# Performance work log

Measured on AMD Instinct MI355X. Metric: run time of the kernel, lower is better.

The kernel has to match this reference:

```python
import jax, jax.numpy as jnp
import numpy as np

MAX_SEQ_LEN = 8192
B, S, D = 4, 8192, 1024
H = 4  # attention heads
N_LEVELS = 3  # levels 1..3 actually occur in the lattice


def _build_spine(max_seq_len):
    spine = [0, 2, 4]
    while True:
        nv = 2 * spine[-1] + 2 * spine[-2] + 2 * spine[-3]
        if nv >= max_seq_len:
            break
        spine.append(nv)
    return spine


def _anc(spine, pos):
    # 3 immediate ancestors from the recurrence (only defined for spine idx >= 3)
    if pos in spine:
        i = spine.index(pos)
        if i >= 3:
            return [spine[i - 1], spine[i - 2], spine[i - 3]]
    return []


def _build_lattice(max_seq_len, seq_len):
    """Static lattice: per spine position, per level, (node indices, path-count weights)."""
    spine = _build_spine(max_seq_len)
    out = []
    for p in spine:
        if p < 3 or p >= seq_len:
            continue
        visited = {p}
        cur = [p]
        levels = {}
        lvl = 0
        while cur and lvl < 10:
            levels[lvl] = list(cur)
            nxt = set()
            for n in cur:
                for a in _anc(spine, n):
                    if a not in visited and a >= 0:
                        visited.add(a)
                        nxt.add(a)
            cur = sorted(nxt)
            lvl += 1
        max_depth = lvl - 1
        # path counts: #paths from p to each ancestor; deepest level pinned to 1 (as in source)
        pc = {p: 1}
        for L in range(1, max_depth + 1):
            for n in levels[L]:
                if L == max_depth:
                    pc[n] = 1
                else:
                    pc[n] = sum(pc.get(c, 0) for c in levels[L - 1] if n in _anc(spine, c))
        entries = []
        for L in range(1, max_depth + 1):
            nodes = [n for n in levels[L] if n < seq_len]
            if nodes:
                entries.append((L, np.asarray(nodes, np.int32),
                                np.asarray([pc.get(n, 1) for n in nodes], np.float32)))
        if entries:
            out.append((p, entries))
    return out


LATTICE = _build_lattice(MAX_SEQ_LEN, S)


def _ln(v, g, b, eps=1e-5):
    mu = jnp.mean(v, axis=-1, keepdims=True)
    var = jnp.mean((v - mu) ** 2, axis=-1, keepdims=True)
    return (v - mu) / jnp.sqrt(var + eps) * g + b


def setup_inputs() -> dict:
    key = jax.random.key(0)
    ks = jax.random.split(key, 10)
    s = 0.02
    return {
        "x": jax.random.normal(ks[0], (B, S, D), jnp.float32),
        # per-level MLP (levels 1..3), stacked: Linear -> LayerNorm -> GELU -> Linear
        "lt_w1": jax.random.normal(ks[1], (N_LEVELS, D, D), jnp.float32) * s,
        "lt_b1": jnp.zeros((N_LEVELS, D), jnp.float32),
        "lt_ln_g": jnp.ones((N_LEVELS, D), jnp.float32),
        "lt_ln_b": jnp.zeros((N_LEVELS, D), jnp.float32),
        "lt_w2": jax.random.normal(ks[2], (N_LEVELS, D, D), jnp.float32) * s,
        "lt_b2": jnp.zeros((N_LEVELS, D), jnp.float32),
        # MultiheadAttention (torch layout): in_proj [3D,D], out_proj [D,D]
        "attn_in_w": jax.random.normal(ks[3], (3 * D, D), jnp.float32) * s,
        "attn_in_b": jnp.zeros((3 * D,), jnp.float32),
        "attn_out_w": jax.random.normal(ks[4], (D, D), jnp.float32) * s,
        "attn_out_b": jnp.zeros((D,), jnp.float32),
        # fusion: Linear(2D->D) + LayerNorm
        "fus_w": jax.random.normal(ks[5], (D, 2 * D), jnp.float32) * s,
        "fus_b": jnp.zeros((D,), jnp.float32),
        "fus_ln_g": jnp.ones((D,), jnp.float32),
        "fus_ln_b": jnp.zeros((D,), jnp.float32),
    }


def reference(x, lt_w1, lt_b1, lt_ln_g, lt_ln_b, lt_w2, lt_b2,
              attn_in_w, attn_in_b, attn_out_w, attn_out_b,
              fus_w, fus_b, fus_ln_g, fus_ln_b):
    Bq, Sq, Dm = x.shape
    hd = Dm // H
    Wq, Wk, Wv = jnp.split(attn_in_w, 3, axis=0)
    bq, bk, bv = jnp.split(attn_in_b, 3)
    pos_list, upds = [], []
    for pos, entries in LATTICE:  # 7 static spine positions
        feats = []
        for (L, nodes, w) in entries:  # <=3 levels, <=3 nodes each
            g = x[:, jnp.asarray(nodes), :]                       # [B,k,D] gather
            wa = jnp.asarray(w)
            f = jnp.einsum('bkd,k->bd', g, wa) / wa.sum()          # weighted mean
            i = L - 1
            h = f @ lt_w1[i].T + lt_b1[i]
            h = _ln(h, lt_ln_g[i], lt_ln_b[i])
            h = jax.nn.gelu(h, approximate=False)
            feats.append(h @ lt_w2[i].T + lt_b2[i])
        kv = jnp.stack(feats, axis=1)                              # [B,L,D]
        q = x[:, pos]                                              # [B,D]
        qh = (q @ Wq.T + bq).reshape(Bq, H, hd)
        kh = (kv @ Wk.T + bk).reshape(Bq, -1, H, hd)
        vh = (kv @ Wv.T + bv).reshape(Bq, -1, H, hd)
        scores = jnp.einsum('bhd,blhd->bhl', qh, kh) / jnp.sqrt(jnp.float32(hd))
        att = jax.nn.softmax(scores, axis=-1)
        o = jnp.einsum('bhl,blhd->bhd', att, vh).reshape(Bq, Dm)
        o = o @ attn_out_w.T + attn_out_b
        comb = jnp.concatenate([o, q], axis=-1)                    # [B,2D]
        upds.append(_ln(comb @ fus_w.T + fus_b, fus_ln_g, fus_ln_b))
        pos_list.append(pos)
    # single scatter of all updated spine positions
    return x.at[:, jnp.asarray(pos_list, jnp.int32), :].set(jnp.stack(upds, axis=1))
```

## Files before the change

kernel.cpp:

```cpp
#include <hip/hip_runtime.h>
#include <math.h>


#define SEQ 8192
#define DM  1024

typedef float fx4 __attribute__((ext_vector_type(4)));

__device__ __constant__ int c_nodes[16][3] = {
  {0,2,4},{2,4,12},{4,12,36},{12,36,104},{36,104,304},{104,304,888},{304,888,2592},
  {0,0,0},{0,2,0},{0,2,4},{2,4,12},{4,12,36},{12,36,104},
  {0,0,0},{0,2,0},{0,2,4}};
__device__ __constant__ float c_wt[16][3] = {
  {1,1,1},{1,1,1},{1,1,1},{1,1,1},{1,1,1},{1,1,1},{1,1,1},
  {1,0,0},{1,1,0},{1,1,1},{1,2,3},{1,2,3},{1,2,3},
  {1,0,0},{1,1,0},{1,1,1}};
__device__ __constant__ float c_winv[16] = {
  1.f/3.f,1.f/3.f,1.f/3.f,1.f/3.f,1.f/3.f,1.f/3.f,1.f/3.f,
  1.f,0.5f,1.f/3.f,1.f/6.f,1.f/6.f,1.f/6.f,
  1.f,0.5f,1.f/3.f};
__device__ __constant__ int c_pos[7]  = {12,36,104,304,888,2592,7568};
__device__ __constant__ int c_ne[7]   = {1,2,2,2,3,3,3};
__device__ __constant__ int c_posE[7][3] = {
  {0,0,0},{1,7,0},{2,8,0},{3,9,0},{4,10,13},{5,11,14},{6,12,15}};

__device__ __constant__ int c_lr0[9]  = {0,8,16,24,28,36,44,52,60};
__device__ __constant__ int c_lnr[9]  = {8,8,8,4,8,8,8,8,4};
__device__ __constant__ int c_llv[9]  = {0,0,0,0,1,1,1,2,2};
__device__ __constant__ int c_or0[4]  = {0,8,16,24};
__device__ __constant__ int c_onr[4]  = {8,8,8,4};

__device__ __forceinline__ void copy4(const float* __restrict__ x,
                                      float* __restrict__ out, int c0)
{
  const fx4* __restrict__ src4 = (const fx4*)x;
  fx4* __restrict__ dst4 = (fx4*)out;
  const int tid = threadIdx.x;
  fx4 v[16]; size_t idx[16];
#pragma unroll
  for (int u = 0; u < 16; ++u) {
    const int c = c0 + (u >> 2), k = u & 3;
    idx[u] = (size_t)c * 1024 + (size_t)k * 256 + tid;
    v[u] = src4[idx[u]];
  }
#pragma unroll
  for (int u = 0; u < 16; ++u) {
    const int s = ((c0 + (u >> 2)) * 4 + (u & 3)) & (SEQ - 1);
    if (s==12 || s==36 || s==104 || s==304 || s==888 || s==2592 || s==7568)
      continue;
    __builtin_nontemporal_store(v[u], &dst4[idx[u]]);
  }
}

__device__ __forceinline__ void acc8(float (&A)[4][8],
                                     const float* const (&Xr)[8],
                                     const float* __restrict__ W,
                                     int Wld, int wcol, int j0, int T)
{
  const int lane = threadIdx.x & 63;
  for (int t = 0; t < T; ++t) {
    const int k = t * 256 + lane * 4;
    const float* wp = W + (size_t)j0 * Wld + wcol + k;
    const float4 w0 = *(const float4*)(wp);
    const float4 w1 = *(const float4*)(wp + Wld);
    const float4 w2 = *(const float4*)(wp + 2 * Wld);
    const float4 w3 = *(const float4*)(wp + 3 * Wld);
#pragma unroll
    for (int r = 0; r < 8; ++r) {
      const float4 xv = *(const float4*)(Xr[r] + k);
      A[0][r] += w0.x*xv.x + w0.y*xv.y + w0.z*xv.z + w0.w*xv.w;
      A[1][r] += w1.x*xv.x + w1.y*xv.y + w1.z*xv.z + w1.w*xv.w;
      A[2][r] += w2.x*xv.x + w2.y*xv.y + w2.z*xv.z + w2.w*xv.w;
      A[3][r] += w3.x*xv.x + w3.y*xv.y + w3.z*xv.z + w3.w*xv.w;
    }
  }
}

__device__ __forceinline__ void fin8(float (&A)[4][8],
                                     const float* __restrict__ Bv, int j0,
                                     float* __restrict__ Y, int ldy,
                                     int r0, int nr)
{
  const int lane = threadIdx.x & 63;
#pragma unroll
  for (int r = 0; r < 8; ++r) {
    float v0 = A[0][r], v1 = A[1][r], v2 = A[2][r], v3 = A[3][r];
#pragma unroll
    for (int off = 32; off >= 1; off >>= 1) {
      v0 += __shfl_xor(v0, off); v1 += __shfl_xor(v1, off);
      v2 += __shfl_xor(v2, off); v3 += __shfl_xor(v3, off);
    }
    if (lane == 0 && r < nr) {
      float* yr = Y + (size_t)(r0 + r) * ldy + j0;
      yr[0] = v0 + Bv[j0];     yr[1] = v1 + Bv[j0 + 1];
      yr[2] = v2 + Bv[j0 + 2]; yr[3] = v3 + Bv[j0 + 3];
    }
  }
}

__global__ __launch_bounds__(256)
void k_feats(const float* __restrict__ x, float* __restrict__ F,
             float* __restrict__ out)
{
  const int bid = blockIdx.x;
  if (bid >= 64) { copy4(x, out, 0 + (bid - 64) * 4); return; }
  const int e = bid >> 2, b = bid & 3;
  const int d = threadIdx.x * 4;
  float4 s = make_float4(0.f, 0.f, 0.f, 0.f);
#pragma unroll
  for (int n = 0; n < 3; ++n) {
    const float w = c_wt[e][n];
    const float4 v = *(const float4*)(x + ((size_t)b*SEQ + c_nodes[e][n])*DM + d);
    s.x += w*v.x; s.y += w*v.y; s.z += w*v.z; s.w += w*v.w;
  }
  const float inv = c_winv[e];
  s.x*=inv; s.y*=inv; s.z*=inv; s.w*=inv;
  *(float4*)(F + (size_t)bid*DM + d) = s;
}

__global__ __launch_bounds__(256)
void k_lat1(const float* __restrict__ x, const float* __restrict__ F,
            const float* __restrict__ w1, const float* __restrict__ b1,
            float* __restrict__ Hh, float* __restrict__ out)
{
  const int bid = blockIdx.x;
  if (bid >= 576) { copy4(x, out, 1040 + (bid - 576) * 4); return; }
  const int ch = bid >> 6, jt = bid & 63;
  const int r0 = c_lr0[ch], nr = c_lnr[ch], lvl = c_llv[ch];
  const int j0 = jt * 16 + (threadIdx.x >> 6) * 4;
  float A[4][8] = {};
  const float* Xr[8];
#pragma unroll
  for (int r = 0; r < 8; ++r)
    Xr[r] = F + (size_t)(r0 + ((r < nr) ? r : nr - 1)) * DM;
  acc8(A, Xr, w1 + (size_t)lvl*DM*DM, DM, 0, j0, 4);
  fin8(A, b1 + lvl*DM, j0, Hh, DM, r0, nr);
}

__global__ __launch_bounds__(256)
void k_ln(const float* __restrict__ x, const float* __restrict__ Hh,
          const float* __restrict__ lng, const float* __restrict__ lnb,
          float* __restrict__ G, float* __restrict__ out)
{
  __shared__ float s1[4], s2[4];
  const int bid = blockIdx.x;
  if (bid >= 64) { copy4(x, out, 1960 + (bid - 64) * 4); return; }
  const int lvl = (bid < 28) ? 0 : ((bid < 52) ? 1 : 2);
  const int j = threadIdx.x * 4;
  const int lane = threadIdx.x & 63, wv = threadIdx.x >> 6;
  const float4 v = *(const float4*)(Hh + (size_t)bid*DM + j);
  float s = v.x+v.y+v.z+v.w;
  float q = v.x*v.x+v.y*v.y+v.z*v.z+v.w*v.w;
#pragma unroll
  for (int off = 32; off >= 1; off >>= 1) {
    s += __shfl_xor(s, off); q += __shfl_xor(q, off);
  }
  if (lane == 0) { s1[wv] = s; s2[wv] = q; }
  __syncthreads();
  const float ts = s1[0]+s1[1]+s1[2]+s1[3];
  const float tq = s2[0]+s2[1]+s2[2]+s2[3];
  const float m = ts * (1.f/1024.f);
  const float rs = rsqrtf(tq * (1.f/1024.f) - m*m + 1e-5f);
  const float4 g4 = *(const float4*)(lng + (size_t)lvl*DM + j);
  const float4 b4 = *(const float4*)(lnb + (size_t)lvl*DM + j);
  const float t0 = (v.x-m)*rs*g4.x + b4.x;
  const float t1 = (v.y-m)*rs*g4.y + b4.y;
  const float t2 = (v.z-m)*rs*g4.z + b4.z;
  const float t3 = (v.w-m)*rs*g4.w + b4.w;
  const float kc = 0.70710678118654752f;
  float4 o;
  o.x = 0.5f*t0*(1.f+erff(t0*kc));
  o.y = 0.5f*t1*(1.f+erff(t1*kc));
  o.z = 0.5f*t2*(1.f+erff(t2*kc));
  o.w = 0.5f*t3*(1.f+erff(t3*kc));
  *(float4*)(G + (size_t)bid*DM + j) = o;
}

__global__ __launch_bounds__(256)
void k_lat2(const float* __restrict__ x, const float* __restrict__ G,
            const float* __restrict__ w2, const float* __restrict__ b2,
            float* __restrict__ KV, float* __restrict__ out)
{
  const int bid = blockIdx.x;
  if (bid >= 576) { copy4(x, out, 3080 + (bid - 576) * 4); return; }
  const int ch = bid >> 6, jt = bid & 63;
  const int r0 = c_lr0[ch], nr = c_lnr[ch], lvl = c_llv[ch];
  const int j0 = jt * 16 + (threadIdx.x >> 6) * 4;
  float A[4][8] = {};
  const float* Xr[8];
#pragma unroll
  for (int r = 0; r < 8; ++r)
    Xr[r] = G + (size_t)(r0 + ((r < nr) ? r : nr - 1)) * DM;
  acc8(A, Xr, w2 + (size_t)lvl*DM*DM, DM, 0, j0, 4);
  fin8(A, b2 + lvl*DM, j0, KV, DM, r0, nr);
}

__global__ __launch_bounds__(256)
void k_qkv(const float* __restrict__ x, const float* __restrict__ KV,
           const float* __restrict__ Wi, const float* __restrict__ Bi,
           float* __restrict__ QH, float* __restrict__ KH,
           float* __restrict__ VH, float* __restrict__ out)
{
  const int bid = blockIdx.x;
  if (bid >= 1280) { copy4(x, out, 4000 + (bid - 1280) * 4); return; }
  const int ch = bid >> 6, jt = bid & 63;
  const int j0 = jt * 16 + (threadIdx.x >> 6) * 4;
  float A[4][8] = {};
  const float* Xr[8];
  if (ch < 4) {
    const int r0 = c_or0[ch], nr = c_onr[ch];
#pragma unroll
    for (int r = 0; r < 8; ++r) {
      const int i = r0 + ((r < nr) ? r : nr - 1);
      Xr[r] = x + ((size_t)(i & 3)*SEQ + c_pos[i >> 2])*DM;
    }
    acc8(A, Xr, Wi, DM, 0, j0, 4);
    fin8(A, Bi, j0, QH, DM, r0, nr);
  } else if (ch < 12) {
    const int r0 = (ch - 4) * 8;
#pragma unroll
    for (int r = 0; r < 8; ++r) Xr[r] = KV + (size_t)(r0 + r)*DM;
    acc8(A, Xr, Wi + (size_t)DM*DM, DM, 0, j0, 4);
    fin8(A, Bi + DM, j0, KH, DM, r0, 8);
  } else {
    const int r0 = (ch - 12) * 8;
#pragma unroll
    for (int r = 0; r < 8; ++r) Xr[r] = KV + (size_t)(r0 + r)*DM;
    acc8(A, Xr, Wi + (size_t)2*DM*DM, DM, 0, j0, 4);
    fin8(A, Bi + 2*DM, j0, VH, DM, r0, 8);
  }
}

__global__ __launch_bounds__(256)
void k_attn(const float* __restrict__ x, const float* __restrict__ QH,
            const float* __restrict__ KH, const float* __restrict__ VH,
            float* __restrict__ OA, float* __restrict__ out)
{
  const int bid = blockIdx.x;
  if (bid >= 28) { copy4(x, out, 4512 + (bid - 28) * 4); return; }
  const int p = bid >> 2, b = bid & 3;
  const int h = threadIdx.x >> 6, lane = threadIdx.x & 63;
  const int ne = c_ne[p];
  const int qoff = (p*4+b)*DM + h*256 + lane;
  const float q0 = QH[qoff], q1 = QH[qoff+64], q2 = QH[qoff+128], q3 = QH[qoff+192];
  float sc0 = -1e30f, sc1 = -1e30f, sc2 = -1e30f;
  int k0 = 0, k1 = 0, k2 = 0;
  {
    k0 = (c_posE[p][0]*4 + b)*DM + h*256 + lane;
    float pr = q0*KH[k0] + q1*KH[k0+64] + q2*KH[k0+128] + q3*KH[k0+192];
#pragma unroll
    for (int off = 32; off >= 1; off >>= 1) pr += __shfl_xor(pr, off);
    sc0 = pr * 0.0625f;
  }
  if (ne > 1) {
    k1 = (c_posE[p][1]*4 + b)*DM + h*256 + lane;
    float pr = q0*KH[k1] + q1*KH[k1+64] + q2*KH[k1+128] + q3*KH[k1+192];
#pragma unroll
    for (int off = 32; off >= 1; off >>= 1) pr += __shfl_xor(pr, off);
    sc1 = pr * 0.0625f;
  }
  if (ne > 2) {
    k2 = (c_posE[p][2]*4 + b)*DM + h*256 + lane;
    float pr = q0*KH[k2] + q1*KH[k2+64] + q2*KH[k2+128] + q3*KH[k2+192];
#pragma unroll
    for (int off = 32; off >= 1; off >>= 1) pr += __shfl_xor(pr, off);
    sc2 = pr * 0.0625f;
  }
  const float m = fmaxf(sc0, fmaxf(sc1, sc2));
  const float e0 = expf(sc0 - m);
  const float e1 = (ne > 1) ? expf(sc1 - m) : 0.f;
  const float e2 = (ne > 2) ? expf(sc2 - m) : 0.f;
  const float inv = 1.f / (e0 + e1 + e2);
  const float A0 = e0*inv, A1 = e1*inv, A2 = e2*inv;
#pragma unroll
  for (int i = 0; i < 4; ++i) {
    float o = A0 * VH[k0 + i*64];
    if (ne > 1) o += A1 * VH[k1 + i*64];
    if (ne > 2) o += A2 * VH[k2 + i*64];
    OA[qoff + i*64] = o;
  }
}

__global__ __launch_bounds__(256)
void k_oproj(const float* __restrict__ x, const float* __restrict__ OA,
             const float* __restrict__ Wo, const float* __restrict__ Bo,
             float* __restrict__ O, float* __restrict__ out)
{
  const int bid = blockIdx.x;
  if (bid >= 256) { copy4(x, out, 5712 + (bid - 256) * 4); return; }
  const int ch = bid >> 6, jt = bid & 63;
  const int r0 = c_or0[ch], nr = c_onr[ch];
  const int j0 = jt * 16 + (threadIdx.x >> 6) * 4;
  float A[4][8] = {};
  const float* Xr[8];
#pragma unroll
  for (int r = 0; r < 8; ++r)
    Xr[r] = OA + (size_t)(r0 + ((r < nr) ? r : nr - 1)) * DM;
  acc8(A, Xr, Wo, DM, 0, j0, 4);
  fin8(A, Bo, j0, O, DM, r0, nr);
}

__global__ __launch_bounds__(256)
void k_fus(const float* __restrict__ x, const float* __restrict__ O,
           const float* __restrict__ Wf, const float* __restrict__ Bf,
           float* __restrict__ UP, float* __restrict__ out)
{
  const int bid = blockIdx.x;
  if (bid >= 256) { copy4(x, out, 6712 + (bid - 256) * 4); return; }
  const int ch = bid >> 6, jt = bid & 63;
  const int r0 = c_or0[ch], nr = c_onr[ch];
  const int j0 = jt * 16 + (threadIdx.x >> 6) * 4;
  float A[4][8] = {};
  const float* XrO[8]; const float* XrX[8];
#pragma unroll
  for (int r = 0; r < 8; ++r) {
    const int i = r0 + ((r < nr) ? r : nr - 1);
    XrO[r] = O + (size_t)i*DM;
    XrX[r] = x + ((size_t)(i & 3)*SEQ + c_pos[i >> 2])*DM;
  }
  acc8(A, XrO, Wf, 2048, 0, j0, 4);
  acc8(A, XrX, Wf, 2048, 1024, j0, 4);
  fin8(A, Bf, j0, UP, DM, r0, nr);
}

__global__ __launch_bounds__(256)
void k_final(const float* __restrict__ x, const float* __restrict__ UP,
             const float* __restrict__ g, const float* __restrict__ bt,
             float* __restrict__ out)
{
  __shared__ float s1[4], s2[4];
  const int bid = blockIdx.x;
  if (bid >= 28) { copy4(x, out, 7712 + (bid - 28) * 4); return; }
  const int p = bid >> 2, b = bid & 3;
  const int j = threadIdx.x * 4;
  const int lane = threadIdx.x & 63, wv = threadIdx.x >> 6;
  const float4 v = *(const float4*)(UP + (size_t)bid*DM + j);
  float s = v.x+v.y+v.z+v.w;
  float q = v.x*v.x+v.y*v.y+v.z*v.z+v.w*v.w;
#pragma unroll
  for (int off = 32; off >= 1; off >>= 1) {
    s += __shfl_xor(s, off); q += __shfl_xor(q, off);
  }
  if (lane == 0) { s1[wv] = s; s2[wv] = q; }
  __syncthreads();
  const float ts = s1[0]+s1[1]+s1[2]+s1[3];
  const float tq = s2[0]+s2[1]+s2[2]+s2[3];
  const float m = ts * (1.f/1024.f);
  const float rs = rsqrtf(tq * (1.f/1024.f) - m*m + 1e-5f);
  const float* gg = g + j;
  const float* bb = bt + j;
  float4 o;
  o.x = (v.x-m)*rs*gg[0] + bb[0];
  o.y = (v.y-m)*rs*gg[1] + bb[1];
  o.z = (v.z-m)*rs*gg[2] + bb[2];
  o.w = (v.w-m)*rs*gg[3] + bb[3];
  *(float4*)(out + ((size_t)b*SEQ + c_pos[p])*DM + j) = o;
}

extern "C" void kernel_launch(void* const* d_in, const int* in_sizes, int n_in,
                              void* d_out, int out_size, void* d_ws, size_t ws_size,
                              hipStream_t stream)
{
  const float* x          = (const float*)d_in[0];
  const float* lt_w1      = (const float*)d_in[1];
  const float* lt_b1      = (const float*)d_in[2];
  const float* lt_ln_g    = (const float*)d_in[3];
  const float* lt_ln_b    = (const float*)d_in[4];
  const float* lt_w2      = (const float*)d_in[5];
  const float* lt_b2      = (const float*)d_in[6];
  const float* attn_in_w  = (const float*)d_in[7];
  const float* attn_in_b  = (const float*)d_in[8];
  const float* attn_out_w = (const float*)d_in[9];
  const float* attn_out_b = (const float*)d_in[10];
  const float* fus_w      = (const float*)d_in[11];
  const float* fus_b      = (const float*)d_in[12];
  const float* fus_ln_g   = (const float*)d_in[13];
  const float* fus_ln_b   = (const float*)d_in[14];
  float* out = (float*)d_out;
  float* ws  = (float*)d_ws;

  float* F  = ws;
  float* Hh = F  + 65536;
  float* G  = Hh + 65536;
  float* KV = G  + 65536;
  float* QH = KV + 65536;
  float* KH = QH + 32768;
  float* VH = KH + 65536;
  float* OA = VH + 65536;
  float* O  = OA + 32768;
  float* UP = O  + 32768;

  k_feats<<<324,  256, 0, stream>>>(x, F, out);
  k_lat1 <<<806,  256, 0, stream>>>(x, F, lt_w1, lt_b1, Hh, out);
  k_ln   <<<344,  256, 0, stream>>>(x, Hh, lt_ln_g, lt_ln_b, G, out);
  k_lat2 <<<806,  256, 0, stream>>>(x, G, lt_w2, lt_b2, KV, out);
  k_qkv  <<<1408, 256, 0, stream>>>(x, KV, attn_in_w, attn_in_b, QH, KH, VH, out);
  k_attn <<<328,  256, 0, stream>>>(x, QH, KH, VH, OA, out);
  k_oproj<<<506,  256, 0, stream>>>(x, OA, attn_out_w, attn_out_b, O, out);
  k_fus  <<<506,  256, 0, stream>>>(x, O, fus_w, fus_b, UP, out);
  k_final<<<148,  256, 0, stream>>>(x, UP, fus_ln_g, fus_ln_b, out);
}
```

Before: 100.1 us.

## Fuse feature gather and LayerNorm/GELU into GEMV kernels, widen row tiles to 16

The weighted-mean feature gather moves into k_lat1 and the LayerNorm+GELU into k_lat2, both staging the input rows in shared memory, which removes two kernel launches and their intermediate buffers. The qkv, out-projection and fusion GEMVs now process 16 rows per block instead of 8, using offset tables, so each weight row is read from global memory half as many times. The copy-block ranges are rebalanced across the remaining seven launches. In exchange, the 16-row accumulators raise register pressure, and the serialized per-row LayerNorm with two barriers per row adds latency inside k_lat2.

```diff
diff --git a/kernel.cpp b/kernel.cpp
--- a/kernel.cpp
+++ b/kernel.cpp
@@ -27,8 +27,30 @@
 __device__ __constant__ int c_lr0[9]  = {0,8,16,24,28,36,44,52,60};
 __device__ __constant__ int c_lnr[9]  = {8,8,8,4,8,8,8,8,4};
 __device__ __constant__ int c_llv[9]  = {0,0,0,0,1,1,1,2,2};
-__device__ __constant__ int c_or0[4]  = {0,8,16,24};
-__device__ __constant__ int c_onr[4]  = {8,8,8,4};
+
+__device__ __constant__ int c_qoff[28] = {
+    12288,  8400896, 16789504, 25178112,
+    36864,  8425472, 16814080, 25202688,
+   106496,  8495104, 16883712, 25272320,
+   311296,  8699904, 17088512, 25477120,
+   909312,  9297920, 17686528, 26075136,
+  2654208, 11042816, 19431424, 27820032,
+  7749632, 16138240, 24526848, 32915456};
+
+__device__ __constant__ int c_lin[64] = {
+      0,  1024,  2048,  3072,  4096,  5120,  6144,  7168,
+   8192,  9216, 10240, 11264, 12288, 13312, 14336, 15360,
+  16384, 17408, 18432, 19456, 20480, 21504, 22528, 23552,
+  24576, 25600, 26624, 27648, 28672, 29696, 30720, 31744,
+  32768, 33792, 34816, 35840, 36864, 37888, 38912, 39936,
+  40960, 41984, 43008, 44032, 45056, 46080, 47104, 48128,
+  49152, 50176, 51200, 52224, 53248, 54272, 55296, 56320,
+  57344, 58368, 59392, 60416, 61440, 62464, 63488, 64512};
+
+__device__ __constant__ int c_q16r0[10] = {0,16, 0,16,32,48, 0,16,32,48};
+__device__ __constant__ int c_q16nr[10] = {16,12,16,16,16,16,16,16,16,16};
+__device__ __constant__ int c_o16r0[2]  = {0,16};
+__device__ __constant__ int c_o16nr[2]  = {16,12};
 
 __device__ __forceinline__ void copy4(const float* __restrict__ x,
                                       float* __restrict__ out, int c0)
@@ -52,10 +74,12 @@
   }
 }
 
-__device__ __forceinline__ void acc8(float (&A)[4][8],
-                                     const float* const (&Xr)[8],
-                                     const float* __restrict__ W,
-                                     int Wld, int wcol, int j0, int T)
+__device__ __forceinline__ void acc16(float (&A)[4][16],
+                                      const float* __restrict__ X,
+                                      const int* __restrict__ off,
+                                      int r0, int nr,
+                                      const float* __restrict__ W,
+                                      int Wld, int wcol, int j0, int T)
 {
   const int lane = threadIdx.x & 63;
   for (int t = 0; t < T; ++t) {
@@ -66,8 +90,9 @@
     const float4 w2 = *(const float4*)(wp + 2 * Wld);
     const float4 w3 = *(const float4*)(wp + 3 * Wld);
 #pragma unroll
-    for (int r = 0; r < 8; ++r) {
-      const float4 xv = *(const float4*)(Xr[r] + k);
+    for (int r = 0; r < 16; ++r) {
+      const int rr = (r < nr) ? r : nr - 1;
+      const float4 xv = *(const float4*)(X + off[r0 + rr] + k);
       A[0][r] += w0.x*xv.x + w0.y*xv.y + w0.z*xv.z + w0.w*xv.w;
       A[1][r] += w1.x*xv.x + w1.y*xv.y + w1.z*xv.z + w1.w*xv.w;
       A[2][r] += w2.x*xv.x + w2.y*xv.y + w2.z*xv.z + w2.w*xv.w;
@@ -76,14 +101,14 @@
   }
 }
 
-__device__ __forceinline__ void fin8(float (&A)[4][8],
-                                     const float* __restrict__ Bv, int j0,
-                                     float* __restrict__ Y, int ldy,
-                                     int r0, int nr)
+__device__ __forceinline__ void fin16(float (&A)[4][16],
+                                      const float* __restrict__ Bv, int j0,
+                                      float* __restrict__ Y, int ldy,
+                                      int r0, int nr)
 {
   const int lane = threadIdx.x & 63;
 #pragma unroll
-  for (int r = 0; r < 8; ++r) {
+  for (int r = 0; r < 16; ++r) {
     float v0 = A[0][r], v1 = A[1][r], v2 = A[2][r], v3 = A[3][r];
 #pragma unroll
     for (int off = 32; off >= 1; off >>= 1) {
@@ -98,101 +123,130 @@
   }
 }
 
-__global__ __launch_bounds__(256)
-void k_feats(const float* __restrict__ x, float* __restrict__ F,
-             float* __restrict__ out)
-{
-  const int bid = blockIdx.x;
-  if (bid >= 64) { copy4(x, out, 0 + (bid - 64) * 4); return; }
-  const int e = bid >> 2, b = bid & 3;
-  const int d = threadIdx.x * 4;
-  float4 s = make_float4(0.f, 0.f, 0.f, 0.f);
-#pragma unroll
-  for (int n = 0; n < 3; ++n) {
-    const float w = c_wt[e][n];
-    const float4 v = *(const float4*)(x + ((size_t)b*SEQ + c_nodes[e][n])*DM + d);
-    s.x += w*v.x; s.y += w*v.y; s.z += w*v.z; s.w += w*v.w;
-  }
-  const float inv = c_winv[e];
-  s.x*=inv; s.y*=inv; s.z*=inv; s.w*=inv;
-  *(float4*)(F + (size_t)bid*DM + d) = s;
-}
-
-__global__ __launch_bounds__(256)
-void k_lat1(const float* __restrict__ x, const float* __restrict__ F,
-            const float* __restrict__ w1, const float* __restrict__ b1,
-            float* __restrict__ Hh, float* __restrict__ out)
-{
-  const int bid = blockIdx.x;
-  if (bid >= 576) { copy4(x, out, 1040 + (bid - 576) * 4); return; }
+__device__ __forceinline__ void acc8_lds(float (&A)[4][8],
+                                         const float (*Xs)[1024], int nr,
+                                         const float* __restrict__ W,
+                                         int j0)
+{
+  const int lane = threadIdx.x & 63;
+  for (int t = 0; t < 4; ++t) {
+    const int k = t * 256 + lane * 4;
+    const float* wp = W + (size_t)j0 * DM + k;
+    const float4 w0 = *(const float4*)(wp);
+    const float4 w1 = *(const float4*)(wp + DM);
+    const float4 w2 = *(const float4*)(wp + 2 * DM);
+    const float4 w3 = *(const float4*)(wp + 3 * DM);
+#pragma unroll
+    for (int r = 0; r < 8; ++r) {
+      const int rc = (r < nr) ? r : nr - 1;
+      const float4 xv = *(const float4*)(&Xs[rc][k]);
+      A[0][r] += w0.x*xv.x + w0.y*xv.y + w0.z*xv.z + w0.w*xv.w;
+      A[1][r] += w1.x*xv.x + w1.y*xv.y + w1.z*xv.z + w1.w*xv.w;
+      A[2][r] += w2.x*xv.x + w2.y*xv.y + w2.z*xv.z + w2.w*xv.w;
+      A[3][r] += w3.x*xv.x + w3.y*xv.y + w3.z*xv.z + w3.w*xv.w;
+    }
+  }
+}
+
+__device__ __forceinline__ void fin8(float (&A)[4][8],
+                                     const float* __restrict__ Bv, int j0,
+                                     float* __restrict__ Y,
+                                     int r0, int nr)
+{
+  const int lane = threadIdx.x & 63;
+#pragma unroll
+  for (int r = 0; r < 8; ++r) {
+    float v0 = A[0][r], v1 = A[1][r], v2 = A[2][r], v3 = A[3][r];
+#pragma unroll
+    for (int off = 32; off >= 1; off >>= 1) {
+      v0 += __shfl_xor(v0, off); v1 += __shfl_xor(v1, off);
+      v2 += __shfl_xor(v2, off); v3 += __shfl_xor(v3, off);
+    }
+    if (lane == 0 && r < nr) {
+      float* yr = Y + (size_t)(r0 + r) * DM + j0;
+      yr[0] = v0 + Bv[j0];     yr[1] = v1 + Bv[j0 + 1];
+      yr[2] = v2 + Bv[j0 + 2]; yr[3] = v3 + Bv[j0 + 3];
+    }
+  }
+}
+
+__global__ __launch_bounds__(256)
+void k_lat1(const float* __restrict__ x, const float* __restrict__ w1,
+            const float* __restrict__ b1, float* __restrict__ Hh,
+            float* __restrict__ out)
+{
+  __shared__ float Xs[8][1024];
+  const int bid = blockIdx.x;
+  if (bid >= 576) { copy4(x, out, 0 + (bid - 576) * 4); return; }
   const int ch = bid >> 6, jt = bid & 63;
   const int r0 = c_lr0[ch], nr = c_lnr[ch], lvl = c_llv[ch];
-  const int j0 = jt * 16 + (threadIdx.x >> 6) * 4;
+  const int tid = threadIdx.x;
+  for (int rr = 0; rr < nr; ++rr) {
+    const int row = r0 + rr, e = row >> 2, b = row & 3;
+    float4 s = make_float4(0.f, 0.f, 0.f, 0.f);
+#pragma unroll
+    for (int n = 0; n < 3; ++n) {
+      const float w = c_wt[e][n];
+      const float4 v = *(const float4*)(x + ((size_t)b*SEQ + c_nodes[e][n])*DM + tid*4);
+      s.x += w*v.x; s.y += w*v.y; s.z += w*v.z; s.w += w*v.w;
+    }
+    const float inv = c_winv[e];
+    *(float4*)&Xs[rr][tid*4] = make_float4(s.x*inv, s.y*inv, s.z*inv, s.w*inv);
+  }
+  __syncthreads();
+  const int j0 = jt * 16 + (tid >> 6) * 4;
   float A[4][8] = {};
-  const float* Xr[8];
-#pragma unroll
-  for (int r = 0; r < 8; ++r)
-    Xr[r] = F + (size_t)(r0 + ((r < nr) ? r : nr - 1)) * DM;
-  acc8(A, Xr, w1 + (size_t)lvl*DM*DM, DM, 0, j0, 4);
-  fin8(A, b1 + lvl*DM, j0, Hh, DM, r0, nr);
-}
-
-__global__ __launch_bounds__(256)
-void k_ln(const float* __restrict__ x, const float* __restrict__ Hh,
-          const float* __restrict__ lng, const float* __restrict__ lnb,
-          float* __restrict__ G, float* __restrict__ out)
-{
-  __shared__ float s1[4], s2[4];
-  const int bid = blockIdx.x;
-  if (bid >= 64) { copy4(x, out, 1960 + (bid - 64) * 4); return; }
-  const int lvl = (bid < 28) ? 0 : ((bid < 52) ? 1 : 2);
-  const int j = threadIdx.x * 4;
-  const int lane = threadIdx.x & 63, wv = threadIdx.x >> 6;
-  const float4 v = *(const float4*)(Hh + (size_t)bid*DM + j);
-  float s = v.x+v.y+v.z+v.w;
-  float q = v.x*v.x+v.y*v.y+v.z*v.z+v.w*v.w;
-#pragma unroll
-  for (int off = 32; off >= 1; off >>= 1) {
-    s += __shfl_xor(s, off); q += __shfl_xor(q, off);
-  }
-  if (lane == 0) { s1[wv] = s; s2[wv] = q; }
-  __syncthreads();
-  const float ts = s1[0]+s1[1]+s1[2]+s1[3];
-  const float tq = s2[0]+s2[1]+s2[2]+s2[3];
-  const float m = ts * (1.f/1024.f);
-  const float rs = rsqrtf(tq * (1.f/1024.f) - m*m + 1e-5f);
-  const float4 g4 = *(const float4*)(lng + (size_t)lvl*DM + j);
-  const float4 b4 = *(const float4*)(lnb + (size_t)lvl*DM + j);
-  const float t0 = (v.x-m)*rs*g4.x + b4.x;
-  const float t1 = (v.y-m)*rs*g4.y + b4.y;
-  const float t2 = (v.z-m)*rs*g4.z + b4.z;
-  const float t3 = (v.w-m)*rs*g4.w + b4.w;
-  const float kc = 0.70710678118654752f;
-  float4 o;
-  o.x = 0.5f*t0*(1.f+erff(t0*kc));
-  o.y = 0.5f*t1*(1.f+erff(t1*kc));
-  o.z = 0.5f*t2*(1.f+erff(t2*kc));
-  o.w = 0.5f*t3*(1.f+erff(t3*kc));
-  *(float4*)(G + (size_t)bid*DM + j) = o;
-}
-
-__global__ __launch_bounds__(256)
-void k_lat2(const float* __restrict__ x, const float* __restrict__ G,
+  acc8_lds(A, Xs, nr, w1 + (size_t)lvl*DM*DM, j0);
+  fin8(A, b1 + lvl*DM, j0, Hh, r0, nr);
+}
+
+__global__ __launch_bounds__(256)
+void k_lat2(const float* __restrict__ x, const float* __restrict__ Hh,
+            const float* __restrict__ lng, const float* __restrict__ lnb,
             const float* __restrict__ w2, const float* __restrict__ b2,
             float* __restrict__ KV, float* __restrict__ out)
 {
-  const int bid = blockIdx.x;
-  if (bid >= 576) { copy4(x, out, 3080 + (bid - 576) * 4); return; }
+  __shared__ float Xs[8][1024];
+  __shared__ float s1[4], s2[4];
+  const int bid = blockIdx.x;
+  if (bid >= 576) { copy4(x, out, 1100 + (bid - 576) * 4); return; }
   const int ch = bid >> 6, jt = bid & 63;
   const int r0 = c_lr0[ch], nr = c_lnr[ch], lvl = c_llv[ch];
-  const int j0 = jt * 16 + (threadIdx.x >> 6) * 4;
+  const int tid = threadIdx.x;
+  const int lane = tid & 63, wv = tid >> 6;
+  const float4 g4 = *(const float4*)(lng + (size_t)lvl*DM + tid*4);
+  const float4 b4 = *(const float4*)(lnb + (size_t)lvl*DM + tid*4);
+  for (int rr = 0; rr < nr; ++rr) {
+    const float4 v = *(const float4*)(Hh + (size_t)(r0+rr)*DM + tid*4);
+    float s = v.x+v.y+v.z+v.w;
+    float q = v.x*v.x+v.y*v.y+v.z*v.z+v.w*v.w;
+#pragma unroll
+    for (int off = 32; off >= 1; off >>= 1) {
+      s += __shfl_xor(s, off); q += __shfl_xor(q, off);
+    }
+    if (lane == 0) { s1[wv] = s; s2[wv] = q; }
+    __syncthreads();
+    const float ts = s1[0]+s1[1]+s1[2]+s1[3];
+    const float tq = s2[0]+s2[1]+s2[2]+s2[3];
+    const float m = ts * (1.f/1024.f);
+    const float rs = rsqrtf(tq * (1.f/1024.f) - m*m + 1e-5f);
+    const float t0 = (v.x-m)*rs*g4.x + b4.x;
+    const float t1 = (v.y-m)*rs*g4.y + b4.y;
+    const float t2 = (v.z-m)*rs*g4.z + b4.z;
+    const float t3 = (v.w-m)*rs*g4.w + b4.w;
+    const float kc = 0.70710678118654752f;
+    float4 o;
+    o.x = 0.5f*t0*(1.f+erff(t0*kc));
+    o.y = 0.5f*t1*(1.f+erff(t1*kc));
+    o.z = 0.5f*t2*(1.f+erff(t2*kc));
+    o.w = 0.5f*t3*(1.f+erff(t3*kc));
+    *(float4*)&Xs[rr][tid*4] = o;
+    __syncthreads();
+  }
+  const int j0 = jt * 16 + wv * 4;
   float A[4][8] = {};
-  const float* Xr[8];
-#pragma unroll
-  for (int r = 0; r < 8; ++r)
-    Xr[r] = G + (size_t)(r0 + ((r < nr) ? r : nr - 1)) * DM;
-  acc8(A, Xr, w2 + (size_t)lvl*DM*DM, DM, 0, j0, 4);
-  fin8(A, b2 + lvl*DM, j0, KV, DM, r0, nr);
+  acc8_lds(A, Xs, nr, w2 + (size_t)lvl*DM*DM, j0);
+  fin8(A, b2 + lvl*DM, j0, KV, r0, nr);
 }
 
 __global__ __launch_bounds__(256)
@@ -202,32 +256,20 @@
            float* __restrict__ VH, float* __restrict__ out)
 {
   const int bid = blockIdx.x;
-  if (bid >= 1280) { copy4(x, out, 4000 + (bid - 1280) * 4); return; }
+  if (bid >= 640) { copy4(x, out, 2200 + (bid - 640) * 4); return; }
   const int ch = bid >> 6, jt = bid & 63;
+  const int r0 = c_q16r0[ch], nr = c_q16nr[ch];
   const int j0 = jt * 16 + (threadIdx.x >> 6) * 4;
-  float A[4][8] = {};
-  const float* Xr[8];
-  if (ch < 4) {
-    const int r0 = c_or0[ch], nr = c_onr[ch];
-#pragma unroll
-    for (int r = 0; r < 8; ++r) {
-      const int i = r0 + ((r < nr) ? r : nr - 1);
-      Xr[r] = x + ((size_t)(i & 3)*SEQ + c_pos[i >> 2])*DM;
-    }
-    acc8(A, Xr, Wi, DM, 0, j0, 4);
-    fin8(A, Bi, j0, QH, DM, r0, nr);
-  } else if (ch < 12) {
-    const int r0 = (ch - 4) * 8;
-#pragma unroll
-    for (int r = 0; r < 8; ++r) Xr[r] = KV + (size_t)(r0 + r)*DM;
-    acc8(A, Xr, Wi + (size_t)DM*DM, DM, 0, j0, 4);
-    fin8(A, Bi + DM, j0, KH, DM, r0, 8);
+  float A[4][16] = {};
+  if (ch < 2) {
+    acc16(A, x, c_qoff, r0, nr, Wi, DM, 0, j0, 4);
+    fin16(A, Bi, j0, QH, DM, r0, nr);
+  } else if (ch < 6) {
+    acc16(A, KV, c_lin, r0, nr, Wi + (size_t)DM*DM, DM, 0, j0, 4);
+    fin16(A, Bi + DM, j0, KH, DM, r0, nr);
   } else {
-    const int r0 = (ch - 12) * 8;
-#pragma unroll
-    for (int r = 0; r < 8; ++r) Xr[r] = KV + (size_t)(r0 + r)*DM;
-    acc8(A, Xr, Wi + (size_t)2*DM*DM, DM, 0, j0, 4);
-    fin8(A, Bi + 2*DM, j0, VH, DM, r0, 8);
+    acc16(A, KV, c_lin, r0, nr, Wi + (size_t)2*DM*DM, DM, 0, j0, 4);
+    fin16(A, Bi + 2*DM, j0, VH, DM, r0, nr);
   }
 }
 
@@ -237,7 +279,7 @@
             float* __restrict__ OA, float* __restrict__ out)
 {
   const int bid = blockIdx.x;
-  if (bid >= 28) { copy4(x, out, 4512 + (bid - 28) * 4); return; }
+  if (bid >= 28) { copy4(x, out, 3300 + (bid - 28) * 4); return; }
   const int p = bid >> 2, b = bid & 3;
   const int h = threadIdx.x >> 6, lane = threadIdx.x & 63;
   const int ne = c_ne[p];
@@ -287,17 +329,13 @@
              float* __restrict__ O, float* __restrict__ out)
 {
   const int bid = blockIdx.x;
-  if (bid >= 256) { copy4(x, out, 5712 + (bid - 256) * 4); return; }
+  if (bid >= 128) { copy4(x, out, 4700 + (bid - 128) * 4); return; }
   const int ch = bid >> 6, jt = bid & 63;
-  const int r0 = c_or0[ch], nr = c_onr[ch];
+  const int r0 = c_o16r0[ch], nr = c_o16nr[ch];
   const int j0 = jt * 16 + (threadIdx.x >> 6) * 4;
-  float A[4][8] = {};
-  const float* Xr[8];
-#pragma unroll
-  for (int r = 0; r < 8; ++r)
-    Xr[r] = OA + (size_t)(r0 + ((r < nr) ? r : nr - 1)) * DM;
-  acc8(A, Xr, Wo, DM, 0, j0, 4);
-  fin8(A, Bo, j0, O, DM, r0, nr);
+  float A[4][16] = {};
+  acc16(A, OA, c_lin, r0, nr, Wo, DM, 0, j0, 4);
+  fin16(A, Bo, j0, O, DM, r0, nr);
 }
 
 __global__ __launch_bounds__(256)
@@ -306,21 +344,14 @@
            float* __restrict__ UP, float* __restrict__ out)
 {
   const int bid = blockIdx.x;
-  if (bid >= 256) { copy4(x, out, 6712 + (bid - 256) * 4); return; }
+  if (bid >= 128) { copy4(x, out, 6000 + (bid - 128) * 4); return; }
   const int ch = bid >> 6, jt = bid & 63;
-  const int r0 = c_or0[ch], nr = c_onr[ch];
+  const int r0 = c_o16r0[ch], nr = c_o16nr[ch];
   const int j0 = jt * 16 + (threadIdx.x >> 6) * 4;
-  float A[4][8] = {};
-  const float* XrO[8]; const float* XrX[8];
-#pragma unroll
-  for (int r = 0; r < 8; ++r) {
-    const int i = r0 + ((r < nr) ? r : nr - 1);
-    XrO[r] = O + (size_t)i*DM;
-    XrX[r] = x + ((size_t)(i & 3)*SEQ + c_pos[i >> 2])*DM;
-  }
-  acc8(A, XrO, Wf, 2048, 0, j0, 4);
-  acc8(A, XrX, Wf, 2048, 1024, j0, 4);
-  fin8(A, Bf, j0, UP, DM, r0, nr);
+  float A[4][16] = {};
+  acc16(A, O, c_lin,  r0, nr, Wf, 2048, 0,    j0, 4);
+  acc16(A, x, c_qoff, r0, nr, Wf, 2048, 1024, j0, 4);
+  fin16(A, Bf, j0, UP, DM, r0, nr);
 }
 
 __global__ __launch_bounds__(256)
@@ -330,7 +361,7 @@
 {
   __shared__ float s1[4], s2[4];
   const int bid = blockIdx.x;
-  if (bid >= 28) { copy4(x, out, 7712 + (bid - 28) * 4); return; }
+  if (bid >= 28) { copy4(x, out, 7200 + (bid - 28) * 4); return; }
   const int p = bid >> 2, b = bid & 3;
   const int j = threadIdx.x * 4;
   const int lane = threadIdx.x & 63, wv = threadIdx.x >> 6;
@@ -379,10 +410,8 @@
   float* out = (float*)d_out;
   float* ws  = (float*)d_ws;
 
-  float* F  = ws;
-  float* Hh = F  + 65536;
-  float* G  = Hh + 65536;
-  float* KV = G  + 65536;
+  float* Hh = ws;
+  float* KV = Hh + 65536;
   float* QH = KV + 65536;
   float* KH = QH + 32768;
   float* VH = KH + 65536;
@@ -390,13 +419,11 @@
   float* O  = OA + 32768;
   float* UP = O  + 32768;
 
-  k_feats<<<324,  256, 0, stream>>>(x, F, out);
-  k_lat1 <<<806,  256, 0, stream>>>(x, F, lt_w1, lt_b1, Hh, out);
-  k_ln   <<<344,  256, 0, stream>>>(x, Hh, lt_ln_g, lt_ln_b, G, out);
-  k_lat2 <<<806,  256, 0, stream>>>(x, G, lt_w2, lt_b2, KV, out);
-  k_qkv  <<<1408, 256, 0, stream>>>(x, KV, attn_in_w, attn_in_b, QH, KH, VH, out);
-  k_attn <<<328,  256, 0, stream>>>(x, QH, KH, VH, OA, out);
-  k_oproj<<<506,  256, 0, stream>>>(x, OA, attn_out_w, attn_out_b, O, out);
-  k_fus  <<<506,  256, 0, stream>>>(x, O, fus_w, fus_b, UP, out);
-  k_final<<<148,  256, 0, stream>>>(x, UP, fus_ln_g, fus_ln_b, out);
-}
+  k_lat1 <<<851, 256, 0, stream>>>(x, lt_w1, lt_b1, Hh, out);
+  k_lat2 <<<851, 256, 0, stream>>>(x, Hh, lt_ln_g, lt_ln_b, lt_w2, lt_b2, KV, out);
+  k_qkv  <<<915, 256, 0, stream>>>(x, KV, attn_in_w, attn_in_b, QH, KH, VH, out);
+  k_attn <<<378, 256, 0, stream>>>(x, QH, KH, VH, OA, out);
+  k_oproj<<<453, 256, 0, stream>>>(x, OA, attn_out_w, attn_out_b, O, out);
+  k_fus  <<<428, 256, 0, stream>>>(x, O, fus_w, fus_b, UP, out);
+  k_final<<<276, 256, 0, stream>>>(x, UP, fus_ln_g, fus_ln_b, out);
+}
```

Result: slower. 120.9 us (+20.9%).

## Loop over row chunks inside GEMV blocks to cut redundant weight reads

Applied to the files above, without the earlier changes.

Each GEMM kernel previously launched one block per (row-chunk, column-tile), so each weight column tile was re-read from memory once per row chunk. Now one block per column tile (and per level or matrix) loops over all row chunks, so the weight tile is read by a single block and is likely to stay in cache across iterations. The copy-block offsets for the passthrough of x are rebalanced to match the smaller grids. The trade-off is far fewer compute blocks (64 to 192 per kernel), which lowers parallelism and lengthens the serial loop in each block.

```diff
diff --git a/kernel.cpp b/kernel.cpp
--- a/kernel.cpp
+++ b/kernel.cpp
@@ -26,7 +26,6 @@
 
 __device__ __constant__ int c_lr0[9]  = {0,8,16,24,28,36,44,52,60};
 __device__ __constant__ int c_lnr[9]  = {8,8,8,4,8,8,8,8,4};
-__device__ __constant__ int c_llv[9]  = {0,0,0,0,1,1,1,2,2};
 __device__ __constant__ int c_or0[4]  = {0,8,16,24};
 __device__ __constant__ int c_onr[4]  = {8,8,8,4};
 
@@ -124,17 +123,23 @@
             float* __restrict__ Hh, float* __restrict__ out)
 {
   const int bid = blockIdx.x;
-  if (bid >= 576) { copy4(x, out, 1040 + (bid - 576) * 4); return; }
-  const int ch = bid >> 6, jt = bid & 63;
-  const int r0 = c_lr0[ch], nr = c_lnr[ch], lvl = c_llv[ch];
+  if (bid >= 192) { copy4(x, out, 1040 + (bid - 192) * 4); return; }
+  const int lvl = bid >> 6, jt = bid & 63;
   const int j0 = jt * 16 + (threadIdx.x >> 6) * 4;
-  float A[4][8] = {};
-  const float* Xr[8];
-#pragma unroll
-  for (int r = 0; r < 8; ++r)
-    Xr[r] = F + (size_t)(r0 + ((r < nr) ? r : nr - 1)) * DM;
-  acc8(A, Xr, w1 + (size_t)lvl*DM*DM, DM, 0, j0, 4);
-  fin8(A, b1 + lvl*DM, j0, Hh, DM, r0, nr);
+  const float* W = w1 + (size_t)lvl * DM * DM;
+  const float* Bv = b1 + lvl * DM;
+  const int chlo = (lvl == 0) ? 0 : ((lvl == 1) ? 4 : 7);
+  const int chhi = (lvl == 0) ? 4 : ((lvl == 1) ? 7 : 9);
+  for (int ch = chlo; ch < chhi; ++ch) {
+    const int r0 = c_lr0[ch], nr = c_lnr[ch];
+    float A[4][8] = {};
+    const float* Xr[8];
+#pragma unroll
+    for (int r = 0; r < 8; ++r)
+      Xr[r] = F + (size_t)(r0 + ((r < nr) ? r : nr - 1)) * DM;
+    acc8(A, Xr, W, DM, 0, j0, 4);
+    fin8(A, Bv, j0, Hh, DM, r0, nr);
+  }
 }
 
 __global__ __launch_bounds__(256)
@@ -182,17 +187,23 @@
             float* __restrict__ KV, float* __restrict__ out)
 {
   const int bid = blockIdx.x;
-  if (bid >= 576) { copy4(x, out, 3080 + (bid - 576) * 4); return; }
-  const int ch = bid >> 6, jt = bid & 63;
-  const int r0 = c_lr0[ch], nr = c_lnr[ch], lvl = c_llv[ch];
+  if (bid >= 192) { copy4(x, out, 3080 + (bid - 192) * 4); return; }
+  const int lvl = bid >> 6, jt = bid & 63;
   const int j0 = jt * 16 + (threadIdx.x >> 6) * 4;
-  float A[4][8] = {};
-  const float* Xr[8];
-#pragma unroll
-  for (int r = 0; r < 8; ++r)
-    Xr[r] = G + (size_t)(r0 + ((r < nr) ? r : nr - 1)) * DM;
-  acc8(A, Xr, w2 + (size_t)lvl*DM*DM, DM, 0, j0, 4);
-  fin8(A, b2 + lvl*DM, j0, KV, DM, r0, nr);
+  const float* W = w2 + (size_t)lvl * DM * DM;
+  const float* Bv = b2 + lvl * DM;
+  const int chlo = (lvl == 0) ? 0 : ((lvl == 1) ? 4 : 7);
+  const int chhi = (lvl == 0) ? 4 : ((lvl == 1) ? 7 : 9);
+  for (int ch = chlo; ch < chhi; ++ch) {
+    const int r0 = c_lr0[ch], nr = c_lnr[ch];
+    float A[4][8] = {};
+    const float* Xr[8];
+#pragma unroll
+    for (int r = 0; r < 8; ++r)
+      Xr[r] = G + (size_t)(r0 + ((r < nr) ? r : nr - 1)) * DM;
+    acc8(A, Xr, W, DM, 0, j0, 4);
+    fin8(A, Bv, j0, KV, DM, r0, nr);
+  }
 }
 
 __global__ __launch_bounds__(256)
@@ -202,32 +213,35 @@
            float* __restrict__ VH, float* __restrict__ out)
 {
   const int bid = blockIdx.x;
-  if (bid >= 1280) { copy4(x, out, 4000 + (bid - 1280) * 4); return; }
-  const int ch = bid >> 6, jt = bid & 63;
+  if (bid >= 192) { copy4(x, out, 4000 + (bid - 192) * 4); return; }
+  const int mat = bid >> 6, jt = bid & 63;
   const int j0 = jt * 16 + (threadIdx.x >> 6) * 4;
-  float A[4][8] = {};
-  const float* Xr[8];
-  if (ch < 4) {
-    const int r0 = c_or0[ch], nr = c_onr[ch];
-#pragma unroll
-    for (int r = 0; r < 8; ++r) {
-      const int i = r0 + ((r < nr) ? r : nr - 1);
-      Xr[r] = x + ((size_t)(i & 3)*SEQ + c_pos[i >> 2])*DM;
-    }
-    acc8(A, Xr, Wi, DM, 0, j0, 4);
-    fin8(A, Bi, j0, QH, DM, r0, nr);
-  } else if (ch < 12) {
-    const int r0 = (ch - 4) * 8;
-#pragma unroll
-    for (int r = 0; r < 8; ++r) Xr[r] = KV + (size_t)(r0 + r)*DM;
-    acc8(A, Xr, Wi + (size_t)DM*DM, DM, 0, j0, 4);
-    fin8(A, Bi + DM, j0, KH, DM, r0, 8);
+  if (mat == 0) {
+    for (int ic = 0; ic < 4; ++ic) {
+      const int r0 = c_or0[ic], nr = c_onr[ic];
+      float A[4][8] = {};
+      const float* Xr[8];
+#pragma unroll
+      for (int r = 0; r < 8; ++r) {
+        const int i = r0 + ((r < nr) ? r : nr - 1);
+        Xr[r] = x + ((size_t)(i & 3)*SEQ + c_pos[i >> 2])*DM;
+      }
+      acc8(A, Xr, Wi, DM, 0, j0, 4);
+      fin8(A, Bi, j0, QH, DM, r0, nr);
+    }
   } else {
-    const int r0 = (ch - 12) * 8;
-#pragma unroll
-    for (int r = 0; r < 8; ++r) Xr[r] = KV + (size_t)(r0 + r)*DM;
-    acc8(A, Xr, Wi + (size_t)2*DM*DM, DM, 0, j0, 4);
-    fin8(A, Bi + 2*DM, j0, VH, DM, r0, 8);
+    const float* W = Wi + (size_t)mat * DM * DM;
+    const float* Bv = Bi + mat * DM;
+    float* Y = (mat == 1) ? KH : VH;
+    for (int ic = 0; ic < 8; ++ic) {
+      const int r0 = ic * 8;
+      float A[4][8] = {};
+      const float* Xr[8];
+#pragma unroll
+      for (int r = 0; r < 8; ++r) Xr[r] = KV + (size_t)(r0 + r)*DM;
+      acc8(A, Xr, W, DM, 0, j0, 4);
+      fin8(A, Bv, j0, Y, DM, r0, 8);
+    }
   }
 }
 
@@ -237,7 +251,7 @@
             float* __restrict__ OA, float* __restrict__ out)
 {
   const int bid = blockIdx.x;
-  if (bid >= 28) { copy4(x, out, 4512 + (bid - 28) * 4); return; }
+  if (bid >= 28) { copy4(x, out, 4912 + (bid - 28) * 4); return; }
   const int p = bid >> 2, b = bid & 3;
   const int h = threadIdx.x >> 6, lane = threadIdx.x & 63;
   const int ne = c_ne[p];
@@ -287,17 +301,18 @@
              float* __restrict__ O, float* __restrict__ out)
 {
   const int bid = blockIdx.x;
-  if (bid >= 256) { copy4(x, out, 5712 + (bid - 256) * 4); return; }
-  const int ch = bid >> 6, jt = bid & 63;
-  const int r0 = c_or0[ch], nr = c_onr[ch];
-  const int j0 = jt * 16 + (threadIdx.x >> 6) * 4;
-  float A[4][8] = {};
-  const float* Xr[8];
-#pragma unroll
-  for (int r = 0; r < 8; ++r)
-    Xr[r] = OA + (size_t)(r0 + ((r < nr) ? r : nr - 1)) * DM;
-  acc8(A, Xr, Wo, DM, 0, j0, 4);
-  fin8(A, Bo, j0, O, DM, r0, nr);
+  if (bid >= 64) { copy4(x, out, 5912 + (bid - 64) * 4); return; }
+  const int j0 = bid * 16 + (threadIdx.x >> 6) * 4;
+  for (int ic = 0; ic < 4; ++ic) {
+    const int r0 = c_or0[ic], nr = c_onr[ic];
+    float A[4][8] = {};
+    const float* Xr[8];
+#pragma unroll
+    for (int r = 0; r < 8; ++r)
+      Xr[r] = OA + (size_t)(r0 + ((r < nr) ? r : nr - 1)) * DM;
+    acc8(A, Xr, Wo, DM, 0, j0, 4);
+    fin8(A, Bo, j0, O, DM, r0, nr);
+  }
 }
 
 __global__ __launch_bounds__(256)
@@ -306,21 +321,22 @@
            float* __restrict__ UP, float* __restrict__ out)
 {
   const int bid = blockIdx.x;
-  if (bid >= 256) { copy4(x, out, 6712 + (bid - 256) * 4); return; }
-  const int ch = bid >> 6, jt = bid & 63;
-  const int r0 = c_or0[ch], nr = c_onr[ch];
-  const int j0 = jt * 16 + (threadIdx.x >> 6) * 4;
-  float A[4][8] = {};
-  const float* XrO[8]; const float* XrX[8];
-#pragma unroll
-  for (int r = 0; r < 8; ++r) {
-    const int i = r0 + ((r < nr) ? r : nr - 1);
-    XrO[r] = O + (size_t)i*DM;
-    XrX[r] = x + ((size_t)(i & 3)*SEQ + c_pos[i >> 2])*DM;
-  }
-  acc8(A, XrO, Wf, 2048, 0, j0, 4);
-  acc8(A, XrX, Wf, 2048, 1024, j0, 4);
-  fin8(A, Bf, j0, UP, DM, r0, nr);
+  if (bid >= 64) { copy4(x, out, 6912 + (bid - 64) * 4); return; }
+  const int j0 = bid * 16 + (threadIdx.x >> 6) * 4;
+  for (int ic = 0; ic < 4; ++ic) {
+    const int r0 = c_or0[ic], nr = c_onr[ic];
+    float A[4][8] = {};
+    const float* XrO[8]; const float* XrX[8];
+#pragma unroll
+    for (int r = 0; r < 8; ++r) {
+      const int i = r0 + ((r < nr) ? r : nr - 1);
+      XrO[r] = O + (size_t)i*DM;
+      XrX[r] = x + ((size_t)(i & 3)*SEQ + c_pos[i >> 2])*DM;
+    }
+    acc8(A, XrO, Wf, 2048, 0, j0, 4);
+    acc8(A, XrX, Wf, 2048, 1024, j0, 4);
+    fin8(A, Bf, j0, UP, DM, r0, nr);
+  }
 }
 
 __global__ __launch_bounds__(256)
@@ -390,13 +406,13 @@
   float* O  = OA + 32768;
   float* UP = O  + 32768;
 
-  k_feats<<<324,  256, 0, stream>>>(x, F, out);
-  k_lat1 <<<806,  256, 0, stream>>>(x, F, lt_w1, lt_b1, Hh, out);
-  k_ln   <<<344,  256, 0, stream>>>(x, Hh, lt_ln_g, lt_ln_b, G, out);
-  k_lat2 <<<806,  256, 0, stream>>>(x, G, lt_w2, lt_b2, KV, out);
-  k_qkv  <<<1408, 256, 0, stream>>>(x, KV, attn_in_w, attn_in_b, QH, KH, VH, out);
-  k_attn <<<328,  256, 0, stream>>>(x, QH, KH, VH, OA, out);
-  k_oproj<<<506,  256, 0, stream>>>(x, OA, attn_out_w, attn_out_b, O, out);
-  k_fus  <<<506,  256, 0, stream>>>(x, O, fus_w, fus_b, UP, out);
-  k_final<<<148,  256, 0, stream>>>(x, UP, fus_ln_g, fus_ln_b, out);
-}
+  k_feats<<<324, 256, 0, stream>>>(x, F, out);
+  k_lat1 <<<422, 256, 0, stream>>>(x, F, lt_w1, lt_b1, Hh, out);
+  k_ln   <<<344, 256, 0, stream>>>(x, Hh, lt_ln_g, lt_ln_b, G, out);
+  k_lat2 <<<422, 256, 0, stream>>>(x, G, lt_w2, lt_b2, KV, out);
+  k_qkv  <<<420, 256, 0, stream>>>(x, KV, attn_in_w, attn_in_b, QH, KH, VH, out);
+  k_attn <<<278, 256, 0, stream>>>(x, QH, KH, VH, OA, out);
+  k_oproj<<<314, 256, 0, stream>>>(x, OA, attn_out_w, attn_out_b, O, out);
+  k_fus  <<<264, 256, 0, stream>>>(x, O, fus_w, fus_b, UP, out);
+  k_final<<<148, 256, 0, stream>>>(x, UP, fus_ln_g, fus_ln_b, out);
+}
```

Result: slower. 186.3 us (+86.2%).
